# Kernel optimization log

Measured on AMD Instinct MI355X. Metric: run time of the kernel, lower is better.

## Reference

```python
import jax, jax.numpy as jnp
import numpy as np

D = 1024
H = 16
HD = D // H
T = 2048
B = 2
HID = 4 * D
EPS = 1e-5


def setup_inputs() -> dict:
    key = jax.random.key(0)
    ks = jax.random.split(key, 8)
    s = lambda fan_in: 1.0 / np.sqrt(fan_in)
    return {
        "x": jax.random.normal(ks[0], (B, T, D), dtype=jnp.float32),
        "ln1_g": jnp.ones((D,), jnp.float32),
        "ln1_b": jnp.zeros((D,), jnp.float32),
        "Wqkv": jax.random.uniform(ks[1], (D, 3 * D), jnp.float32, -s(D), s(D)),
        "bqkv": jnp.zeros((3 * D,), jnp.float32),
        "Wout": jax.random.uniform(ks[2], (D, D), jnp.float32, -s(D), s(D)),
        "bout": jnp.zeros((D,), jnp.float32),
        "ln2_g": jnp.ones((D,), jnp.float32),
        "ln2_b": jnp.zeros((D,), jnp.float32),
        "W1": jax.random.uniform(ks[3], (D, HID), jnp.float32, -s(D), s(D)),
        "b1": jnp.zeros((HID,), jnp.float32),
        "W2": jax.random.uniform(ks[4], (HID, D), jnp.float32, -s(HID), s(HID)),
        "b2": jnp.zeros((D,), jnp.float32),
    }


def _layernorm(h, g, b):
    mu = jnp.mean(h, axis=-1, keepdims=True)
    var = jnp.mean(jnp.square(h - mu), axis=-1, keepdims=True)
    return (h - mu) * jax.lax.rsqrt(var + EPS) * g + b


def reference(x, ln1_g, ln1_b, Wqkv, bqkv, Wout, bout, ln2_g, ln2_b, W1, b1, W2, b2):
    b, t, d = x.shape
    scale = 1.0 / np.sqrt(HD)

    # --- attention (pre-LN) ---
    h = _layernorm(x, ln1_g, ln1_b)
    qkv = h @ Wqkv + bqkv                      # [b, t, 3d]
    q, k, v = jnp.split(qkv, 3, axis=-1)
    q = q.reshape(b, t, H, HD)
    k = k.reshape(b, t, H, HD)
    v = v.reshape(b, t, H, HD)
    scores = jnp.einsum("bqhd,bkhd->bhqk", q, k) * scale  # [b, h, t, t]
    causal = jnp.tril(jnp.ones((t, t), dtype=bool))
    scores = jnp.where(causal, scores, -jnp.inf)
    attn = jax.nn.softmax(scores, axis=-1)
    out = jnp.einsum("bhqk,bkhd->bqhd", attn, v).reshape(b, t, d)
    x = x + (out @ Wout + bout)

    # --- MLP (pre-LN) ---
    h = _layernorm(x, ln2_g, ln2_b)
    h = jax.nn.gelu(h @ W1 + b1, approximate=False)
    x = x + (h @ W2 + b2)
    return x
```

## Files before the change

### kernel.cpp

```cpp
#include <hip/hip_runtime.h>
#include <hip/hip_bf16.h>
#include <math.h>

#define DD 1024
#define TT 2048
#define BB 2
#define HH 16
#define HDIM 64
#define HIDD 4096

typedef __attribute__((ext_vector_type(4))) float f32x4;
typedef __attribute__((ext_vector_type(8))) __bf16 bf16x8;
typedef __attribute__((ext_vector_type(4))) __bf16 bf16x4;

#define MF16 __builtin_amdgcn_mfma_f32_16x16x32_bf16

__device__ __forceinline__ void gload_lds16(const void* g, void* l) {
  __builtin_amdgcn_global_load_lds(
      (const __attribute__((address_space(1))) void*)g,
      (__attribute__((address_space(3))) void*)l, 16, 0, 0);
}

__global__ __launch_bounds__(256) void castT64(const float* __restrict__ W,
                                               __bf16* __restrict__ Wt,
                                               int K, int N) {
  __shared__ float t[64][65];
  const int n0 = blockIdx.x * 64, k0 = blockIdx.y * 64;
#pragma unroll
  for (int e = 0; e < 16; ++e) {
    int idx = e * 256 + threadIdx.x;
    int rr = idx >> 6, cc = idx & 63;
    t[rr][cc] = W[(size_t)(k0 + rr) * N + n0 + cc];
  }
  __syncthreads();
#pragma unroll
  for (int e = 0; e < 16; ++e) {
    int idx = e * 256 + threadIdx.x;
    int rr = idx >> 6, cc = idx & 63;
    Wt[(size_t)(n0 + rr) * K + k0 + cc] = (__bf16)t[cc][rr];
  }
}

__global__ __launch_bounds__(256) void ln_fwd(const float* __restrict__ x,
                                              const float* __restrict__ gamma,
                                              const float* __restrict__ beta,
                                              __bf16* __restrict__ out) {
  const int row = blockIdx.x;
  const int t4 = threadIdx.x;
  const float4 v = reinterpret_cast<const float4*>(x + (size_t)row * DD)[t4];
  float s = v.x + v.y + v.z + v.w;
  float ss = v.x * v.x + v.y * v.y + v.z * v.z + v.w * v.w;
#pragma unroll
  for (int m = 32; m >= 1; m >>= 1) { s += __shfl_xor(s, m); ss += __shfl_xor(ss, m); }
  __shared__ float red[8];
  const int wave = threadIdx.x >> 6, lane = threadIdx.x & 63;
  if (lane == 0) { red[wave] = s; red[4 + wave] = ss; }
  __syncthreads();
  s = red[0] + red[1] + red[2] + red[3];
  ss = red[4] + red[5] + red[6] + red[7];
  const float mu = s * (1.0f / DD);
  const float rs = rsqrtf(ss * (1.0f / DD) - mu * mu + 1e-5f);
  const float4 gm = reinterpret_cast<const float4*>(gamma)[t4];
  const float4 bt = reinterpret_cast<const float4*>(beta)[t4];
  bf16x4 o;
  o[0] = (__bf16)((v.x - mu) * rs * gm.x + bt.x);
  o[1] = (__bf16)((v.y - mu) * rs * gm.y + bt.y);
  o[2] = (__bf16)((v.z - mu) * rs * gm.z + bt.z);
  o[3] = (__bf16)((v.w - mu) * rs * gm.w + bt.w);
  *reinterpret_cast<bf16x4*>(out + (size_t)row * DD + t4 * 4) = o;
}

template <int MODE>
__global__ __launch_bounds__(512, 1) void gemm8(const __bf16* __restrict__ A,
                                                const __bf16* __restrict__ Bt,
                                                const float* __restrict__ bias,
                                                void* __restrict__ out0,
                                                __bf16* __restrict__ q1,
                                                __bf16* __restrict__ q2,
                                                __bf16* __restrict__ q3,
                                                int N, int K, int kchunk) {
  const int tid = threadIdx.x;
  const int wid = tid >> 6, lane = tid & 63;
  const int g = lane >> 4, r = lane & 15;
  const int wrh = wid >> 2;
  const int wc = (wid & 3) * 64;

  int bm, bn, kbase, zz;
  if constexpr (MODE == 3) {
    const int L = blockIdx.x;
    const int xcd = L & 7, idx = L >> 3;
    zz = xcd >> 1;
    bm = (((xcd & 1) << 3) + (idx >> 2)) * 256;
    bn = (idx & 3) * 256;
    kbase = zz * kchunk;
  } else {
    const int gx = gridDim.x;
    const int nwg = gx * gridDim.y;
    const int orig = blockIdx.y * gx + blockIdx.x;
    const int swz = (orig & 7) * (nwg >> 3) + (orig >> 3);
    const int bn4 = swz & 3;
    const int bmt = (swz >> 2) % gx;
    const int bng = (swz >> 2) / gx;
    bm = bmt * 256;
    bn = (bng * 4 + bn4) * 256;
    kbase = 0;
    zz = 0;
  }

  const int NT = kchunk >> 6;
  const __bf16* Asrc = A + (size_t)bm * K + kbase;
  const __bf16* Bsrc = Bt + (size_t)bn * K + kbase;

  __shared__ __bf16 lds[2][4][8192];

  f32x4 acc[8][4] = {};
  bf16x8 bfr[4][2];

  auto STG = [&](int ab, int h, int kt) {
    const __bf16* src = (ab ? Bsrc : Asrc) + (size_t)h * 128 * K;
    char* dst = (char*)&lds[kt & 1][ab * 2 + h][0];
#pragma unroll
    for (int gl = 0; gl < 2; ++gl) {
      const int o = gl * 8192 + wid * 1024 + lane * 16;
      const int row = o >> 7;
      const int cbs = (o & 127) ^ (((row >> 2) & 1) << 5);
      gload_lds16((const char*)src + (size_t)row * (K * 2) + kt * 128 + cbs,
                  dst + gl * 8192 + wid * 1024);
    }
  };
  auto DSA = [&](int s, int mi, int kk) -> bf16x8 {
    return *(const bf16x8*)((const char*)&lds[s][wrh][0] + (mi * 16 + r) * 128 +
                            ((kk * 64 + g * 16) ^ ((r & 4) << 3)));
  };
  auto DSB = [&](int s, int nj, int kk) -> bf16x8 {
    const int rt = wc + nj * 16 + r;
    return *(const bf16x8*)((const char*)&lds[s][2 + (rt >> 7)][0] + (rt & 127) * 128 +
                            ((kk * 64 + g * 16) ^ ((r & 4) << 3)));
  };

#define PH(S, Q, STAGE_STMT, WAIT_STMT)                                        \
  {                                                                            \
    if (Q == 0) {                                                              \
      _Pragma("unroll") for (int nj = 0; nj < 4; ++nj) {                       \
        bfr[nj][0] = DSB(S, nj, 0);                                            \
        bfr[nj][1] = DSB(S, nj, 1);                                            \
      }                                                                        \
    }                                                                          \
    bf16x8 a00 = DSA(S, 2 * Q, 0), a01 = DSA(S, 2 * Q, 1);                     \
    bf16x8 a10 = DSA(S, 2 * Q + 1, 0), a11 = DSA(S, 2 * Q + 1, 1);             \
    STAGE_STMT;                                                                \
    WAIT_STMT;                                                                 \
    __builtin_amdgcn_s_barrier();                                              \
    asm volatile("s_waitcnt lgkmcnt(0)" ::: "memory");                         \
    __builtin_amdgcn_s_setprio(1);                                             \
    _Pragma("unroll") for (int nj = 0; nj < 4; ++nj) {                         \
      acc[2 * Q][nj] = MF16(a00, bfr[nj][0], acc[2 * Q][nj], 0, 0, 0);         \
      acc[2 * Q][nj] = MF16(a01, bfr[nj][1], acc[2 * Q][nj], 0, 0, 0);         \
      acc[2 * Q + 1][nj] = MF16(a10, bfr[nj][0], acc[2 * Q + 1][nj], 0, 0, 0); \
      acc[2 * Q + 1][nj] = MF16(a11, bfr[nj][1], acc[2 * Q + 1][nj], 0, 0, 0); \
    }                                                                          \
    __builtin_amdgcn_s_setprio(0);                                             \
    __builtin_amdgcn_s_barrier();                                              \
  }

  STG(1, 0, 0); STG(1, 1, 0); STG(0, 0, 0); STG(0, 1, 0);
  STG(1, 0, 1); STG(1, 1, 1); STG(0, 0, 1);
  asm volatile("s_waitcnt vmcnt(6)" ::: "memory");
  __builtin_amdgcn_s_barrier();

  const int NI = NT >> 1;
  for (int i = 0; i < NI; ++i) {
    const int k2 = 2 * i + 2, k3 = 2 * i + 3;
    const bool nl = (i + 1 < NI);
    PH(0, 0, { STG(0, 1, 2 * i + 1); }, {});
    PH(0, 1, { if (nl) STG(1, 0, k2); }, {});
    PH(0, 2, { if (nl) STG(1, 1, k2); }, {});
    PH(0, 3, { if (nl) STG(0, 0, k2); },
       { if (nl) asm volatile("s_waitcnt vmcnt(6)" ::: "memory");
         else    asm volatile("s_waitcnt vmcnt(0)" ::: "memory"); });
    PH(1, 0, { if (nl) STG(0, 1, k2); }, {});
    PH(1, 1, { if (nl) STG(1, 0, k3); }, {});
    PH(1, 2, { if (nl) STG(1, 1, k3); }, {});
    PH(1, 3, { if (nl) STG(0, 0, k3); },
       { if (nl) asm volatile("s_waitcnt vmcnt(6)" ::: "memory"); });
  }
#undef PH

  const int row0 = bm + wrh * 128 + g * 4;
  const int col0 = bn + wc + r;
#pragma unroll
  for (int mi = 0; mi < 8; ++mi) {
#pragma unroll
    for (int nj = 0; nj < 4; ++nj) {
      const int col = col0 + nj * 16;
      float bv = 0.0f;
      if constexpr (MODE != 3) bv = bias[col];
#pragma unroll
      for (int i4 = 0; i4 < 4; ++i4) {
        const int rowg = row0 + mi * 16 + i4;
        const size_t idx = (size_t)rowg * N + col;
        const float v = acc[mi][nj][i4];
        if constexpr (MODE == 0) {
          ((__bf16*)out0)[idx] = (__bf16)(v + bv);
        } else if constexpr (MODE == 2) {
          const float t = v + bv;
          const float u2 = t * (1.5957691216f + t * t * 0.0713548163f);
          ((__bf16*)out0)[idx] = (__bf16)(t * __builtin_amdgcn_rcpf(1.0f + __expf(-u2)));
        } else {
          if (zz == 0) {
            ((float*)out0)[idx] = v;
          } else {
            __bf16* p = (zz == 1 ? q1 : (zz == 2 ? q2 : q3));
            p[idx] = (__bf16)v;
          }
        }
      }
    }
  }
}

__global__ __launch_bounds__(256) void reduceW2(const __bf16* __restrict__ p1,
                                                const __bf16* __restrict__ p2,
                                                const __bf16* __restrict__ p3,
                                                const float* __restrict__ x1,
                                                const float* __restrict__ b2,
                                                float* __restrict__ out) {
  const size_t i8 = ((size_t)blockIdx.x * 256 + threadIdx.x) * 8;
  const int col0 = (int)(i8 & 1023);
  bf16x8 a = *(const bf16x8*)(p1 + i8);
  bf16x8 b = *(const bf16x8*)(p2 + i8);
  bf16x8 c = *(const bf16x8*)(p3 + i8);
  float4 o0 = *(const float4*)(out + i8);
  float4 o1 = *(const float4*)(out + i8 + 4);
  const float4 xv0 = *(const float4*)(x1 + i8);
  const float4 xv1 = *(const float4*)(x1 + i8 + 4);
  const float4 bb0 = *(const float4*)(b2 + col0);
  const float4 bb1 = *(const float4*)(b2 + col0 + 4);
  float* op0 = (float*)&o0;
  float* op1 = (float*)&o1;
  const float* xp0 = (const float*)&xv0;
  const float* xp1 = (const float*)&xv1;
  const float* bp0 = (const float*)&bb0;
  const float* bp1 = (const float*)&bb1;
#pragma unroll
  for (int j = 0; j < 4; ++j)
    op0[j] += xp0[j] + bp0[j] + (float)a[j] + (float)b[j] + (float)c[j];
#pragma unroll
  for (int j = 0; j < 4; ++j)
    op1[j] += xp1[j] + bp1[j] + (float)a[4 + j] + (float)b[4 + j] + (float)c[4 + j];
  *(float4*)(out + i8) = o0;
  *(float4*)(out + i8 + 4) = o1;
}

template <int MODE>
__global__ __launch_bounds__(256) void gemm_bt(const __bf16* __restrict__ A,
                                               const __bf16* __restrict__ Bt,
                                               const float* __restrict__ bias,
                                               const float* __restrict__ resid,
                                               void* __restrict__ Cout,
                                               int M, int N, int K) {
  __shared__ __bf16 As[128 * 32];
  __shared__ __bf16 Bs[128 * 32];
  const int tid = threadIdx.x;
  const int wave = tid >> 6, lane = tid & 63;
  const int g = lane >> 4, r = lane & 15;
  const int gx = gridDim.x;
  const int nwg = gx * gridDim.y;
  const int orig = blockIdx.y * gx + blockIdx.x;
  const int swz = (orig & 7) * (nwg >> 3) + (orig >> 3);
  const int bn4 = swz & 3;
  const int bmt = (swz >> 2) % gx;
  const int bng = (swz >> 2) / gx;
  const int bm = bmt * 128;
  const int bn = (bng * 4 + bn4) * 128;
  const int wr = (wave >> 1) * 64, wc = (wave & 1) * 64;
  f32x4 acc[4][4] = {};

  const int off0 = wave * 2048 + lane * 16;
  const int off1 = off0 + 1024;
  const int sr0 = off0 >> 6, sk0 = (off0 & 63) >> 1;
  const int sr1 = off1 >> 6, sk1 = (off1 & 63) >> 1;
  const __bf16* gA0 = A + (size_t)(bm + sr0) * K + sk0;
  const __bf16* gA1 = A + (size_t)(bm + sr1) * K + sk1;
  const __bf16* gB0 = Bt + (size_t)(bn + sr0) * K + sk0;
  const __bf16* gB1 = Bt + (size_t)(bn + sr1) * K + sk1;
  char* lA0 = (char*)As + wave * 2048;
  char* lA1 = lA0 + 1024;
  char* lB0 = (char*)Bs + wave * 2048;
  char* lB1 = lB0 + 1024;

  for (int k0 = 0; k0 < K; k0 += 32) {
    gload_lds16(gA0 + k0, lA0);
    gload_lds16(gA1 + k0, lA1);
    gload_lds16(gB0 + k0, lB0);
    gload_lds16(gB1 + k0, lB1);
    __syncthreads();
    bf16x8 af[4], bf[4];
#pragma unroll
    for (int mi = 0; mi < 4; ++mi)
      af[mi] = *reinterpret_cast<const bf16x8*>(&As[(wr + mi * 16 + r) * 32 + g * 8]);
#pragma unroll
    for (int ni = 0; ni < 4; ++ni)
      bf[ni] = *reinterpret_cast<const bf16x8*>(&Bs[(wc + ni * 16 + r) * 32 + g * 8]);
    __builtin_amdgcn_s_setprio(1);
#pragma unroll
    for (int mi = 0; mi < 4; ++mi)
#pragma unroll
      for (int ni = 0; ni < 4; ++ni)
        acc[mi][ni] = MF16(af[mi], bf[ni], acc[mi][ni], 0, 0, 0);
    __builtin_amdgcn_s_setprio(0);
    __syncthreads();
  }

  const int row0 = bm + wr + 4 * g;
  const int col0 = bn + wc + r;
#pragma unroll
  for (int mi = 0; mi < 4; ++mi) {
#pragma unroll
    for (int ni = 0; ni < 4; ++ni) {
      const int col = col0 + ni * 16;
      const float bv = bias[col];
#pragma unroll
      for (int i = 0; i < 4; ++i) {
        const int row = row0 + mi * 16 + i;
        const size_t idx = (size_t)row * N + col;
        float v = acc[mi][ni][i] + bv;
        if (MODE == 0) {
          ((__bf16*)Cout)[idx] = (__bf16)v;
        } else if (MODE == 1) {
          ((float*)Cout)[idx] = v + resid[idx];
        } else {
          const float u2 = v * (1.5957691216f + v * v * 0.0713548163f);
          const float gl = v * __builtin_amdgcn_rcpf(1.0f + __expf(-u2));
          ((__bf16*)Cout)[idx] = (__bf16)gl;
        }
      }
    }
  }
}

__global__ __launch_bounds__(256) void vtrans(const __bf16* __restrict__ qkv,
                                              __bf16* __restrict__ vtg) {
  const int bh = blockIdx.y, b = bh >> 4, h = bh & 15;
  const int t0 = blockIdx.x * 64;
  const int tid = threadIdx.x, wave = tid >> 6, lane = tid & 63;
  __shared__ __bf16 tile[64 * 64];
#pragma unroll
  for (int e = 0; e < 2; ++e) {
    const int gid = e * 256 + tid;
    const int row = gid >> 3, d0 = (gid & 7) * 8;
    bf16x8 v = *reinterpret_cast<const bf16x8*>(
        qkv + (size_t)(b * TT + t0 + row) * 3072 + 2048 + h * 64 + d0);
    const int slot = (d0 >> 3) ^ (row & 7);
    *reinterpret_cast<bf16x8*>((char*)tile + row * 128 + slot * 16) = v;
  }
  __syncthreads();
  const int d = lane;
#pragma unroll
  for (int e = 0; e < 2; ++e) {
    const int k0 = (wave * 2 + e) * 8;
    bf16x8 o;
#pragma unroll
    for (int j = 0; j < 8; ++j) {
      const int row = k0 + j;
      o[j] = *(const __bf16*)((const char*)tile + row * 128 +
                              (((d >> 3) ^ (row & 7)) << 4) + (d & 7) * 2);
    }
    *reinterpret_cast<bf16x8*>(&vtg[((size_t)bh * 64 + d) * 2048 + t0 + k0]) = o;
  }
}

__device__ __forceinline__ void stage_kv(const __bf16* __restrict__ src_row0, int rstride,
                                         int wave, int lane, char* tile) {
#pragma unroll
  for (int qq = 0; qq < 2; ++qq) {
    const int o = wave * 2048 + qq * 1024 + lane * 16;
    const int p = o >> 12, row = (o >> 6) & 63, cb = (o >> 4) & 3;
    gload_lds16(src_row0 + (size_t)row * rstride + p * 32 + cb * 8,
                tile + wave * 2048 + qq * 1024);
  }
}

__global__ __launch_bounds__(256) void attn_fwd(const __bf16* __restrict__ qkv,
                                                const __bf16* __restrict__ vtg,
                                                __bf16* __restrict__ atto) {
  const int orig = blockIdx.y * gridDim.x + blockIdx.x;
  const int swz = (orig & 7) * 64 + (orig >> 3);
  const int bh = swz >> 4;
  const int j = swz & 15;
  const int b = bh >> 4, h = bh & 15;
  const int tid = threadIdx.x;
  const int wave = tid >> 6, lane = tid & 63;
  const int g = lane >> 4, r = lane & 15;

  __shared__ __bf16 Qs[2 * 64 * 32];
  __shared__ __bf16 Ks[2][2 * 64 * 32];
  __shared__ __bf16 Vs[2][2 * 64 * 32];
  __shared__ __bf16 Pl[4][2 * 16 * 32];

  const __bf16* ksrc = qkv + (size_t)(b * TT) * 3072 + 1024 + h * 64;
  const __bf16* vsrc = vtg + (size_t)bh * 64 * 2048;
  const float C2 = 0.18033688011112042f;

  for (int ph = 0; ph < 2; ++ph) {
    const int qt = ph ? (31 - j) : j;
    const int q0 = qt * 64;
    stage_kv(qkv + (size_t)(b * TT + q0) * 3072 + h * 64, 3072, wave, lane, (char*)Qs);
    stage_kv(ksrc, 3072, wave, lane, (char*)Ks[0]);
    stage_kv(vsrc, 2048, wave, lane, (char*)Vs[0]);

    f32x4 oacc[4] = {};
    float m_s[4], l_s[4];
#pragma unroll
    for (int i = 0; i < 4; ++i) { m_s[i] = -1e30f; l_s[i] = 0.0f; }

    const int nt = qt + 1;
    int cur = 0;
    for (int t = 0; t < nt; ++t) {
      const int kv0 = t * 64;
      __syncthreads();
      if (t + 1 < nt) {
        stage_kv(ksrc + (size_t)(kv0 + 64) * 3072, 3072, wave, lane, (char*)Ks[cur ^ 1]);
        stage_kv(vsrc + kv0 + 64, 2048, wave, lane, (char*)Vs[cur ^ 1]);
      }
      bf16x8 qf[2];
#pragma unroll
      for (int kp = 0; kp < 2; ++kp)
        qf[kp] = *reinterpret_cast<const bf16x8*>(&Qs[kp * 2048 + (wave * 16 + r) * 32 + g * 8]);
      f32x4 s[4];
#pragma unroll
      for (int cn = 0; cn < 4; ++cn) s[cn] = f32x4{0.f, 0.f, 0.f, 0.f};
      __builtin_amdgcn_s_setprio(1);
#pragma unroll
      for (int cn = 0; cn < 4; ++cn)
#pragma unroll
        for (int kp = 0; kp < 2; ++kp) {
          bf16x8 bk = *reinterpret_cast<const bf16x8*>(
              &Ks[cur][kp * 2048 + (cn * 16 + r) * 32 + g * 8]);
          s[cn] = MF16(qf[kp], bk, s[cn], 0, 0, 0);
        }
      __builtin_amdgcn_s_setprio(0);
      const int rowg = q0 + wave * 16 + 4 * g;
      float pm[4];
#pragma unroll
      for (int i = 0; i < 4; ++i) pm[i] = -1e30f;
      if (kv0 + 63 > q0 + wave * 16) {
#pragma unroll
        for (int cn = 0; cn < 4; ++cn) {
          const int colg = kv0 + cn * 16 + r;
#pragma unroll
          for (int i = 0; i < 4; ++i) {
            float v = s[cn][i] * C2;
            v = (colg > rowg + i) ? -1e30f : v;
            s[cn][i] = v;
            pm[i] = fmaxf(pm[i], v);
          }
        }
      } else {
#pragma unroll
        for (int cn = 0; cn < 4; ++cn)
#pragma unroll
          for (int i = 0; i < 4; ++i) {
            const float v = s[cn][i] * C2;
            s[cn][i] = v;
            pm[i] = fmaxf(pm[i], v);
          }
      }
      const int upd = __any((pm[0] > m_s[0] + 8.0f) || (pm[1] > m_s[1] + 8.0f) ||
                            (pm[2] > m_s[2] + 8.0f) || (pm[3] > m_s[3] + 8.0f));
      if (upd) {
#pragma unroll
        for (int i = 0; i < 4; ++i) {
          pm[i] = fmaxf(pm[i], __shfl_xor(pm[i], 1));
          pm[i] = fmaxf(pm[i], __shfl_xor(pm[i], 2));
          pm[i] = fmaxf(pm[i], __shfl_xor(pm[i], 4));
          pm[i] = fmaxf(pm[i], __shfl_xor(pm[i], 8));
          const float mn = fmaxf(m_s[i], pm[i]);
          const float sf = __builtin_amdgcn_exp2f(m_s[i] - mn);
          m_s[i] = mn;
          l_s[i] *= sf;
#pragma unroll
          for (int ni = 0; ni < 4; ++ni) oacc[ni][i] *= sf;
        }
      }
#pragma unroll
      for (int cn = 0; cn < 4; ++cn)
#pragma unroll
        for (int i = 0; i < 4; ++i) {
          const float p = __builtin_amdgcn_exp2f(s[cn][i] - m_s[i]);
          s[cn][i] = p;
          l_s[i] += p;
        }
#pragma unroll
      for (int cn = 0; cn < 4; ++cn)
#pragma unroll
        for (int i = 0; i < 4; ++i) {
          const int row = 4 * g + i;
          const int byteoff = (cn >> 1) * 1024 +
              ((row * 64 + (cn & 1) * 32 + r * 2) ^ ((row & 7) << 4));
          *(__bf16*)((char*)&Pl[wave][0] + byteoff) = (__bf16)s[cn][i];
        }
      bf16x8 pa[2];
#pragma unroll
      for (int kp = 0; kp < 2; ++kp) {
        const int byteoff = kp * 1024 + ((r * 64 + g * 16) ^ ((r & 7) << 4));
        pa[kp] = *reinterpret_cast<const bf16x8*>((const char*)&Pl[wave][0] + byteoff);
      }
      __builtin_amdgcn_s_setprio(1);
#pragma unroll
      for (int ni = 0; ni < 4; ++ni)
#pragma unroll
        for (int kp = 0; kp < 2; ++kp) {
          bf16x8 bv = *reinterpret_cast<const bf16x8*>(
              &Vs[cur][kp * 2048 + (ni * 16 + r) * 32 + g * 8]);
          oacc[ni] = MF16(pa[kp], bv, oacc[ni], 0, 0, 0);
        }
      __builtin_amdgcn_s_setprio(0);
      cur ^= 1;
    }

#pragma unroll
    for (int i = 0; i < 4; ++i) {
      float l = l_s[i];
      l += __shfl_xor(l, 1);
      l += __shfl_xor(l, 2);
      l += __shfl_xor(l, 4);
      l += __shfl_xor(l, 8);
      const float inv = 1.0f / l;
      const size_t rowo = (size_t)(b * TT + q0 + wave * 16 + 4 * g + i) * DD + h * 64;
#pragma unroll
      for (int ni = 0; ni < 4; ++ni)
        atto[rowo + ni * 16 + r] = (__bf16)(oacc[ni][i] * inv);
    }
    __syncthreads();
  }
}

extern "C" void kernel_launch(void* const* d_in, const int* in_sizes, int n_in,
                              void* d_out, int out_size, void* d_ws, size_t ws_size,
                              hipStream_t stream) {
  const float* x     = (const float*)d_in[0];
  const float* ln1_g = (const float*)d_in[1];
  const float* ln1_b = (const float*)d_in[2];
  const float* Wqkv  = (const float*)d_in[3];
  const float* bqkv  = (const float*)d_in[4];
  const float* Wout  = (const float*)d_in[5];
  const float* bout  = (const float*)d_in[6];
  const float* ln2_g = (const float*)d_in[7];
  const float* ln2_b = (const float*)d_in[8];
  const float* W1    = (const float*)d_in[9];
  const float* b1    = (const float*)d_in[10];
  const float* W2    = (const float*)d_in[11];
  const float* b2    = (const float*)d_in[12];
  float* out = (float*)d_out;

  char* ws = (char*)d_ws;
  const size_t MB = 1024 * 1024;
  __bf16* WqkvT = (__bf16*)(ws);
  __bf16* WoutT = (__bf16*)(ws + 6 * MB);
  __bf16* W1T   = (__bf16*)(ws + 8 * MB);
  __bf16* W2T   = (__bf16*)(ws + 16 * MB);
  float*  x1    = (float*)(ws + 24 * MB);
  __bf16* vtg   = (__bf16*)(ws + 24 * MB);
  __bf16* hbuf  = (__bf16*)(ws + 40 * MB);
  __bf16* qkvb  = (__bf16*)(ws + 48 * MB);
  __bf16* atto  = (__bf16*)(ws + 72 * MB);
  __bf16* mlp1  = (__bf16*)(ws + 48 * MB);
  __bf16* p1b   = (__bf16*)(ws);
  __bf16* p2b   = (__bf16*)(ws + 8 * MB);
  __bf16* p3b   = (__bf16*)(ws + 40 * MB);

  castT64<<<dim3(48, 16), 256, 0, stream>>>(Wqkv, WqkvT, 1024, 3072);
  castT64<<<dim3(16, 16), 256, 0, stream>>>(Wout, WoutT, 1024, 1024);
  castT64<<<dim3(64, 16), 256, 0, stream>>>(W1, W1T, 1024, 4096);
  castT64<<<dim3(16, 64), 256, 0, stream>>>(W2, W2T, 4096, 1024);

  ln_fwd<<<4096, 256, 0, stream>>>(x, ln1_g, ln1_b, hbuf);
  gemm8<0><<<dim3(16, 12), 512, 0, stream>>>(hbuf, WqkvT, bqkv, qkvb, nullptr, nullptr, nullptr,
                                             3072, 1024, 1024);
  vtrans<<<dim3(32, 32), 256, 0, stream>>>(qkvb, vtg);
  attn_fwd<<<dim3(16, 32), 256, 0, stream>>>(qkvb, vtg, atto);
  gemm_bt<1><<<dim3(32, 8), 256, 0, stream>>>(atto, WoutT, bout, x, x1, 4096, 1024, 1024);

  ln_fwd<<<4096, 256, 0, stream>>>(x1, ln2_g, ln2_b, hbuf);
  gemm8<2><<<dim3(16, 16), 512, 0, stream>>>(hbuf, W1T, b1, mlp1, nullptr, nullptr, nullptr,
                                             4096, 1024, 1024);
  gemm8<3><<<dim3(256, 1), 512, 0, stream>>>(mlp1, W2T, nullptr, out, p1b, p2b, p3b,
                                             1024, 4096, 1024);
  reduceW2<<<2048, 256, 0, stream>>>(p1b, p2b, p3b, x1, b2, out);
}
```

Before: 240.9 us.

## Merge weight casts, use one wave per LN row, fuse W2 bias+residual

After: 260.3 us. 1.08x slower.

```diff
diff --git a/kernel.cpp b/kernel.cpp
--- a/kernel.cpp
+++ b/kernel.cpp
@@ -21,11 +21,24 @@
       (__attribute__((address_space(3))) void*)l, 16, 0, 0);
 }
 
-__global__ __launch_bounds__(256) void castT64(const float* __restrict__ W,
-                                               __bf16* __restrict__ Wt,
-                                               int K, int N) {
+__global__ __launch_bounds__(256) void castAll(const float* __restrict__ Wqkv,
+                                               const float* __restrict__ Wout,
+                                               const float* __restrict__ W1,
+                                               const float* __restrict__ W2,
+                                               __bf16* __restrict__ WqkvT,
+                                               __bf16* __restrict__ WoutT,
+                                               __bf16* __restrict__ W1T,
+                                               __bf16* __restrict__ W2T) {
+  const int id = blockIdx.x;
+  const float* W;
+  __bf16* Wt;
+  int K, N, gx, local;
+  if (id < 768)        { W = Wqkv; Wt = WqkvT; K = 1024; N = 3072; gx = 48; local = id; }
+  else if (id < 1024)  { W = Wout; Wt = WoutT; K = 1024; N = 1024; gx = 16; local = id - 768; }
+  else if (id < 2048)  { W = W1;   Wt = W1T;   K = 1024; N = 4096; gx = 64; local = id - 1024; }
+  else                 { W = W2;   Wt = W2T;   K = 4096; N = 1024; gx = 16; local = id - 2048; }
+  const int n0 = (local % gx) * 64, k0 = (local / gx) * 64;
   __shared__ float t[64][65];
-  const int n0 = blockIdx.x * 64, k0 = blockIdx.y * 64;
 #pragma unroll
   for (int e = 0; e < 16; ++e) {
     int idx = e * 256 + threadIdx.x;
@@ -45,35 +58,39 @@
                                               const float* __restrict__ gamma,
                                               const float* __restrict__ beta,
                                               __bf16* __restrict__ out) {
-  const int row = blockIdx.x;
-  const int t4 = threadIdx.x;
-  const float4 v = reinterpret_cast<const float4*>(x + (size_t)row * DD)[t4];
-  float s = v.x + v.y + v.z + v.w;
-  float ss = v.x * v.x + v.y * v.y + v.z * v.z + v.w * v.w;
-#pragma unroll
-  for (int m = 32; m >= 1; m >>= 1) { s += __shfl_xor(s, m); ss += __shfl_xor(ss, m); }
-  __shared__ float red[8];
   const int wave = threadIdx.x >> 6, lane = threadIdx.x & 63;
-  if (lane == 0) { red[wave] = s; red[4 + wave] = ss; }
-  __syncthreads();
-  s = red[0] + red[1] + red[2] + red[3];
-  ss = red[4] + red[5] + red[6] + red[7];
+  const int row = blockIdx.x * 4 + wave;
+  const float* xr = x + (size_t)row * DD;
+  float4 v[4];
+  float s = 0.0f, ss = 0.0f;
+#pragma unroll
+  for (int c = 0; c < 4; ++c) {
+    v[c] = reinterpret_cast<const float4*>(xr)[c * 64 + lane];
+    s += v[c].x + v[c].y + v[c].z + v[c].w;
+    ss += v[c].x * v[c].x + v[c].y * v[c].y + v[c].z * v[c].z + v[c].w * v[c].w;
+  }
+#pragma unroll
+  for (int m = 1; m <= 32; m <<= 1) { s += __shfl_xor(s, m); ss += __shfl_xor(ss, m); }
   const float mu = s * (1.0f / DD);
   const float rs = rsqrtf(ss * (1.0f / DD) - mu * mu + 1e-5f);
-  const float4 gm = reinterpret_cast<const float4*>(gamma)[t4];
-  const float4 bt = reinterpret_cast<const float4*>(beta)[t4];
-  bf16x4 o;
-  o[0] = (__bf16)((v.x - mu) * rs * gm.x + bt.x);
-  o[1] = (__bf16)((v.y - mu) * rs * gm.y + bt.y);
-  o[2] = (__bf16)((v.z - mu) * rs * gm.z + bt.z);
-  o[3] = (__bf16)((v.w - mu) * rs * gm.w + bt.w);
-  *reinterpret_cast<bf16x4*>(out + (size_t)row * DD + t4 * 4) = o;
+#pragma unroll
+  for (int c = 0; c < 4; ++c) {
+    const float4 gm = reinterpret_cast<const float4*>(gamma)[c * 64 + lane];
+    const float4 bt = reinterpret_cast<const float4*>(beta)[c * 64 + lane];
+    bf16x4 o;
+    o[0] = (__bf16)((v[c].x - mu) * rs * gm.x + bt.x);
+    o[1] = (__bf16)((v[c].y - mu) * rs * gm.y + bt.y);
+    o[2] = (__bf16)((v[c].z - mu) * rs * gm.z + bt.z);
+    o[3] = (__bf16)((v[c].w - mu) * rs * gm.w + bt.w);
+    *reinterpret_cast<bf16x4*>(out + (size_t)row * DD + (c * 64 + lane) * 4) = o;
+  }
 }
 
 template <int MODE>
 __global__ __launch_bounds__(512, 1) void gemm8(const __bf16* __restrict__ A,
                                                 const __bf16* __restrict__ Bt,
                                                 const float* __restrict__ bias,
+                                                const float* __restrict__ resid,
                                                 void* __restrict__ out0,
                                                 __bf16* __restrict__ q1,
                                                 __bf16* __restrict__ q2,
@@ -195,6 +212,7 @@
       const int col = col0 + nj * 16;
       float bv = 0.0f;
       if constexpr (MODE != 3) bv = bias[col];
+      else if (zz == 0) bv = bias[col];
 #pragma unroll
       for (int i4 = 0; i4 < 4; ++i4) {
         const int rowg = row0 + mi * 16 + i4;
@@ -208,7 +226,7 @@
           ((__bf16*)out0)[idx] = (__bf16)(t * __builtin_amdgcn_rcpf(1.0f + __expf(-u2)));
         } else {
           if (zz == 0) {
-            ((float*)out0)[idx] = v;
+            ((float*)out0)[idx] = v + bv + resid[idx];
           } else {
             __bf16* p = (zz == 1 ? q1 : (zz == 2 ? q2 : q3));
             p[idx] = (__bf16)v;
@@ -222,32 +240,19 @@
 __global__ __launch_bounds__(256) void reduceW2(const __bf16* __restrict__ p1,
                                                 const __bf16* __restrict__ p2,
                                                 const __bf16* __restrict__ p3,
-                                                const float* __restrict__ x1,
-                                                const float* __restrict__ b2,
                                                 float* __restrict__ out) {
   const size_t i8 = ((size_t)blockIdx.x * 256 + threadIdx.x) * 8;
-  const int col0 = (int)(i8 & 1023);
   bf16x8 a = *(const bf16x8*)(p1 + i8);
   bf16x8 b = *(const bf16x8*)(p2 + i8);
   bf16x8 c = *(const bf16x8*)(p3 + i8);
   float4 o0 = *(const float4*)(out + i8);
   float4 o1 = *(const float4*)(out + i8 + 4);
-  const float4 xv0 = *(const float4*)(x1 + i8);
-  const float4 xv1 = *(const float4*)(x1 + i8 + 4);
-  const float4 bb0 = *(const float4*)(b2 + col0);
-  const float4 bb1 = *(const float4*)(b2 + col0 + 4);
   float* op0 = (float*)&o0;
   float* op1 = (float*)&o1;
-  const float* xp0 = (const float*)&xv0;
-  const float* xp1 = (const float*)&xv1;
-  const float* bp0 = (const float*)&bb0;
-  const float* bp1 = (const float*)&bb1;
-#pragma unroll
-  for (int j = 0; j < 4; ++j)
-    op0[j] += xp0[j] + bp0[j] + (float)a[j] + (float)b[j] + (float)c[j];
-#pragma unroll
-  for (int j = 0; j < 4; ++j)
-    op1[j] += xp1[j] + bp1[j] + (float)a[4 + j] + (float)b[4 + j] + (float)c[4 + j];
+#pragma unroll
+  for (int j = 0; j < 4; ++j) op0[j] += (float)a[j] + (float)b[j] + (float)c[j];
+#pragma unroll
+  for (int j = 0; j < 4; ++j) op1[j] += (float)a[4 + j] + (float)b[4 + j] + (float)c[4 + j];
   *(float4*)(out + i8) = o0;
   *(float4*)(out + i8 + 4) = o1;
 }
@@ -570,22 +575,19 @@
   __bf16* p2b   = (__bf16*)(ws + 8 * MB);
   __bf16* p3b   = (__bf16*)(ws + 40 * MB);
 
-  castT64<<<dim3(48, 16), 256, 0, stream>>>(Wqkv, WqkvT, 1024, 3072);
-  castT64<<<dim3(16, 16), 256, 0, stream>>>(Wout, WoutT, 1024, 1024);
-  castT64<<<dim3(64, 16), 256, 0, stream>>>(W1, W1T, 1024, 4096);
-  castT64<<<dim3(16, 64), 256, 0, stream>>>(W2, W2T, 4096, 1024);
-
-  ln_fwd<<<4096, 256, 0, stream>>>(x, ln1_g, ln1_b, hbuf);
-  gemm8<0><<<dim3(16, 12), 512, 0, stream>>>(hbuf, WqkvT, bqkv, qkvb, nullptr, nullptr, nullptr,
-                                             3072, 1024, 1024);
+  castAll<<<3072, 256, 0, stream>>>(Wqkv, Wout, W1, W2, WqkvT, WoutT, W1T, W2T);
+
+  ln_fwd<<<1024, 256, 0, stream>>>(x, ln1_g, ln1_b, hbuf);
+  gemm8<0><<<dim3(16, 12), 512, 0, stream>>>(hbuf, WqkvT, bqkv, nullptr, qkvb,
+                                             nullptr, nullptr, nullptr, 3072, 1024, 1024);
   vtrans<<<dim3(32, 32), 256, 0, stream>>>(qkvb, vtg);
   attn_fwd<<<dim3(16, 32), 256, 0, stream>>>(qkvb, vtg, atto);
   gemm_bt<1><<<dim3(32, 8), 256, 0, stream>>>(atto, WoutT, bout, x, x1, 4096, 1024, 1024);
 
-  ln_fwd<<<4096, 256, 0, stream>>>(x1, ln2_g, ln2_b, hbuf);
-  gemm8<2><<<dim3(16, 16), 512, 0, stream>>>(hbuf, W1T, b1, mlp1, nullptr, nullptr, nullptr,
-                                             4096, 1024, 1024);
-  gemm8<3><<<dim3(256, 1), 512, 0, stream>>>(mlp1, W2T, nullptr, out, p1b, p2b, p3b,
-                                             1024, 4096, 1024);
-  reduceW2<<<2048, 256, 0, stream>>>(p1b, p2b, p3b, x1, b2, out);
-}
+  ln_fwd<<<1024, 256, 0, stream>>>(x1, ln2_g, ln2_b, hbuf);
+  gemm8<2><<<dim3(16, 16), 512, 0, stream>>>(hbuf, W1T, b1, nullptr, mlp1,
+                                             nullptr, nullptr, nullptr, 4096, 1024, 1024);
+  gemm8<3><<<dim3(256, 1), 512, 0, stream>>>(mlp1, W2T, b2, x1, out,
+                                             p1b, p2b, p3b, 1024, 4096, 1024);
+  reduceW2<<<2048, 256, 0, stream>>>(p1b, p2b, p3b, out);
+}
```
